# Performance work log

Measured on AMD Instinct MI355X. Metric: run time of the kernel, lower is better.

## Reference

```python
import jax, jax.numpy as jnp
import numpy as np

N_NODES = 100000
N_EDGES = 1250000
NUM_RELS = 8
D_IN, D_HID, D_OUT = 64, 64, 32


def setup_inputs() -> dict:
    key = jax.random.key(0)
    ks = jax.random.split(key, 10)
    x = jax.random.normal(ks[0], (N_NODES, D_IN), dtype=jnp.float32)
    src = jax.random.randint(ks[1], (N_EDGES,), 0, N_NODES, dtype=jnp.int32)
    dst = jax.random.randint(ks[2], (N_EDGES,), 0, N_NODES, dtype=jnp.int32)
    edge_type = jax.random.randint(ks[3], (N_EDGES,), 0, NUM_RELS, dtype=jnp.int32)
    s1 = 1.0 / np.sqrt(D_IN)
    s2 = 1.0 / np.sqrt(D_HID)
    W1 = jax.random.uniform(ks[4], (NUM_RELS, D_IN, D_HID), jnp.float32, -s1, s1)
    root1 = jax.random.uniform(ks[5], (D_IN, D_HID), jnp.float32, -s1, s1)
    b1 = jnp.zeros((D_HID,), jnp.float32)
    W2 = jax.random.uniform(ks[6], (NUM_RELS, D_HID, D_OUT), jnp.float32, -s2, s2)
    root2 = jax.random.uniform(ks[7], (D_HID, D_OUT), jnp.float32, -s2, s2)
    b2 = jnp.zeros((D_OUT,), jnp.float32)
    return {"x": x, "W1": W1, "root1": root1, "b1": b1,
            "W2": W2, "root2": root2, "b2": b2,
            "src": src, "dst": dst, "edge_type": edge_type}


def rgcn_conv(x, W, root, b, src, dst, edge_type, num_rels, num_nodes):
    # self-loop (root) transform + bias
    out = x @ root + b
    for r in range(num_rels):  # loop over small fixed relation set
        mask = (edge_type == r).astype(x.dtype)          # (E,)
        h = x @ W[r]                                      # (N, dout): transform once per relation
        msg = h[src] * mask[:, None]                      # (E, dout) gather + mask
        agg = jax.ops.segment_sum(msg, dst, num_segments=num_nodes)
        cnt = jax.ops.segment_sum(mask, dst, num_segments=num_nodes)
        out = out + agg / jnp.maximum(cnt, 1.0)[:, None]  # per-relation mean (PyG default aggr)
    return out


def reference(x, W1, root1, b1, W2, root2, b2, src, dst, edge_type):
    h = jax.nn.relu(rgcn_conv(x, W1, root1, b1, src, dst, edge_type, NUM_RELS, N_NODES))
    return rgcn_conv(h, W2, root2, b2, src, dst, edge_type, NUM_RELS, N_NODES)
```

## Files before the change

### kernel.cpp

```cpp
#include <hip/hip_runtime.h>

typedef _Float16 half8 __attribute__((ext_vector_type(8)));
typedef __attribute__((ext_vector_type(4))) float f32x4;

__device__ __forceinline__ unsigned short f2h(float f) {
    _Float16 h = (_Float16)f;
    return *(unsigned short*)&h;
}
__device__ __forceinline__ float h2f(unsigned short u) {
    _Float16 h = *(_Float16*)&u;
    return (float)h;
}


__device__ __forceinline__ void wprep_body(
    const float* __restrict__ W, const float* __restrict__ root,
    unsigned short* __restrict__ wb, int dout, int idx)
{
    int c = idx / (64 * dout);
    int rme = idx % (64 * dout);
    int kk = rme / dout;
    int j = rme % dout;
    float f = (c == 0) ? root[kk * dout + j]
                       : W[(size_t)(c - 1) * 64 * dout + kk * dout + j];
    wb[(size_t)c * dout * 72 + (size_t)j * 72 + kk] = f2h(f);
}

__global__ __launch_bounds__(256) void prep_kernel(
    const float* __restrict__ x, unsigned short* __restrict__ xh, int n8,
    const float* __restrict__ W1, const float* __restrict__ root1,
    unsigned short* __restrict__ wb1,
    const float* __restrict__ W2, const float* __restrict__ root2,
    unsigned short* __restrict__ wb2,
    int* __restrict__ hist, int nhist4)
{
    int id = blockIdx.x * 256 + threadIdx.x;
    if (id < n8) {
        const f32x4* p = (const f32x4*)(x + (size_t)id * 8);
        f32x4 u = p[0], v = p[1];
        half8 o;
#pragma unroll
        for (int j = 0; j < 4; ++j) {
            o[j] = (_Float16)u[j];
            o[j + 4] = (_Float16)v[j];
        }
        *(half8*)(xh + (size_t)id * 8) = o;
        return;
    }
    id -= n8;
    if (id < 9 * 64 * 64) { wprep_body(W1, root1, wb1, 64, id); return; }
    id -= 9 * 64 * 64;
    if (id < 9 * 64 * 32) { wprep_body(W2, root2, wb2, 32, id); return; }
    id -= 9 * 64 * 32;
    if (id < nhist4) ((int4*)hist)[id] = make_int4(0, 0, 0, 0);
}


__global__ __launch_bounds__(256) void hist8_kernel(
    const int* __restrict__ dst, const int* __restrict__ et,
    int* __restrict__ hist, int E)
{
    int e = blockIdx.x * 256 + threadIdx.x;
    if (e < E) atomicAdd(&hist[dst[e] * 8 + et[e]], 1);
}

#define SCAN_TILE 4096
__global__ __launch_bounds__(1024) void scanA_kernel(
    const int* __restrict__ hist, int* __restrict__ bstart,
    int* __restrict__ partial, int nkeys)
{
    __shared__ int wsum[16];
    const int t = threadIdx.x;
    const int lane = t & 63, w = t >> 6;
    const int base = blockIdx.x * SCAN_TILE + t * 4;
    int v[4];
    int s = 0;
#pragma unroll
    for (int i = 0; i < 4; ++i) {
        v[i] = (base + i < nkeys) ? hist[base + i] : 0;
        s += v[i];
    }
    int inc = s;
#pragma unroll
    for (int off = 1; off < 64; off <<= 1) {
        int u = __shfl_up(inc, off);
        if (lane >= off) inc += u;
    }
    if (lane == 63) wsum[w] = inc;
    __syncthreads();
    if (w == 0 && lane < 16) {
        int ws = wsum[lane];
        int winc = ws;
#pragma unroll
        for (int off = 1; off < 16; off <<= 1) {
            int u = __shfl_up(winc, off);
            if (lane >= off) winc += u;
        }
        wsum[lane] = winc - ws;
    }
    __syncthreads();
    int run = wsum[w] + (inc - s);
#pragma unroll
    for (int i = 0; i < 4; ++i) {
        if (base + i < nkeys) bstart[base + i] = run;
        run += v[i];
    }
    if (t == 1023) partial[blockIdx.x] = run;
}

__global__ __launch_bounds__(64) void scanB_kernel(
    const int* __restrict__ partial, int* __restrict__ pscan,
    int* __restrict__ bstart_end, int nblk)
{
    const int lane = threadIdx.x;
    int running = 0;
    for (int b = 0; b < nblk; b += 64) {
        int i = b + lane;
        int o = (i < nblk) ? partial[i] : 0;
        int v = o;
#pragma unroll
        for (int off = 1; off < 64; off <<= 1) {
            int u = __shfl_up(v, off);
            if (lane >= off) v += u;
        }
        if (i < nblk) pscan[i] = running + v - o;
        running += __shfl(v, 63);
    }
    if (lane == 0) *bstart_end = running;
}

__global__ __launch_bounds__(256) void scatter_kernel(
    const int* __restrict__ src, const int* __restrict__ dst,
    const int* __restrict__ et, int* __restrict__ hist,
    const int* __restrict__ bstart, const int* __restrict__ pscan,
    unsigned* __restrict__ srt, int E)
{
    int e = blockIdx.x * 256 + threadIdx.x;
    if (e < E) {
        int key = dst[e] * 8 + et[e];
        int r = atomicSub(&hist[key], 1) - 1;
        srt[bstart[key] + pscan[key >> 12] + r] = (unsigned)src[e];
    }
}


template <int DOUT, int RELU, int OUTH>
__global__ __launch_bounds__(256, 6) void fused_kernel(
    const unsigned short* __restrict__ tab,
    const unsigned* __restrict__ srt,
    const int* __restrict__ bstart,
    const int* __restrict__ pscan,
    const unsigned short* __restrict__ wb,
    const float* __restrict__ bias,
    float* __restrict__ outf,
    unsigned short* __restrict__ outh,
    int n_nodes, int Etot)
{
    __shared__ __align__(16) unsigned short Atile[16 * 600];

    const int t = threadIdx.x;
    const int w = t >> 6, lane = t & 63;
    const int quad = lane >> 4, l16 = lane & 15;
    const int nbt = blockIdx.x * 16;
    const int nb4 = nbt + w * 4;
    const int KEYS = n_nodes * 8;

    {
        const int nb0 = nb4 * 8;
        int idx = nb0 + lane; if (idx > KEYS) idx = KEYS;
        int lv;
        if (idx < KEYS) lv = bstart[idx] + pscan[idx >> 12];
        else            lv = Etot;
        const int E0 = __builtin_amdgcn_readlane(lv, 0);
        const int E1 = __builtin_amdgcn_readlane(lv, 32);

        int cntv = __shfl_down(lv, 1) - lv;
        float rsc = 1.0f / fmaxf((float)cntv, 1.0f);

#pragma unroll
        for (int i = 0; i < 4; ++i) {
            int node = nb4 + i;
            unsigned short v = 0;
            if (node < n_nodes) v = tab[(size_t)node * 64 + lane];
            Atile[(w * 4 + i) * 600 + lane] = v;
        }

        float acc0 = 0.f, acc1 = 0.f;
        int R = 0;
        int bnext = __builtin_amdgcn_readlane(lv, 1);

        auto flushes = [&](int eabs) {
            while (R < 32 && eabs == bnext) {
                float sc = __uint_as_float(
                    __builtin_amdgcn_readlane(__float_as_uint(rsc), R));
                Atile[(w * 4 + (R >> 3)) * 600 + 64 + (R & 7) * 64 + lane] =
                    f2h((acc0 + acc1) * sc);
                acc0 = 0.f; acc1 = 0.f;
                ++R;
                bnext = (R < 31) ? __builtin_amdgcn_readlane(lv, R + 1) : E1;
            }
        };

        const char* tabc = (const char*)tab;
        const unsigned voff = (unsigned)(lane << 1);
        unsigned GA[16], GB[16];

#define ISSUE16(BUF, RECV, KB)                                              \
        _Pragma("unroll")                                                   \
        for (int i_ = 0; i_ < 16; ++i_) {                                   \
            int q_ = __builtin_amdgcn_readlane((int)(RECV), (KB) + i_);     \
            const char* ap_ = tabc + ((size_t)(unsigned)q_ << 7);           \
            asm volatile("global_load_ushort %0, %1, %2"                    \
                         : "=v"(BUF[i_]) : "v"(voff), "s"(ap_));            \
        }
#define WAIT16  asm volatile("s_waitcnt vmcnt(16)" ::: "memory")
#define WAIT0   asm volatile("s_waitcnt vmcnt(0)" ::: "memory")
#define SB      __builtin_amdgcn_sched_barrier(0)
#define CONSUME_FULL(BUF, B)                                                \
        _Pragma("unroll")                                                   \
        for (int i_ = 0; i_ < 16; ++i_) {                                   \
            flushes(base + (B) + i_);                                       \
            if (i_ & 1) acc1 += h2f((unsigned short)BUF[i_]);               \
            else        acc0 += h2f((unsigned short)BUF[i_]);               \
        }
#define CONSUME_TAIL(BUF, B)                                                \
        _Pragma("unroll")                                                   \
        for (int i_ = 0; i_ < 16; ++i_) {                                   \
            if ((B) + i_ < blen) {                                          \
                flushes(base + (B) + i_);                                   \
                if (i_ & 1) acc1 += h2f((unsigned short)BUF[i_]);           \
                else        acc0 += h2f((unsigned short)BUF[i_]);           \
            }                                                               \
        }

        int base = E0;
        unsigned rec = 0;
        if (base < E1 && lane < E1 - base) rec = srt[base + lane];
        while (base < E1) {
            const int blen = min(64, E1 - base);
            const int nbase = base + 64;
            unsigned recn = 0;
            if (nbase < E1) {
                int ei = nbase + lane;
                if (ei > E1 - 1) ei = E1 - 1;
                unsigned eoff = (unsigned)ei << 2;
                asm volatile("global_load_dword %0, %1, %2"
                             : "=v"(recn) : "v"(eoff), "s"(srt));
            }

            const bool m1 = blen > 16, m2 = blen > 32, m3 = blen > 48;
            ISSUE16(GA, rec, 0);
            if (m1) { ISSUE16(GB, rec, 16); WAIT16; } else WAIT0;
            SB;
            if (blen >= 16) { CONSUME_FULL(GA, 0); } else { CONSUME_TAIL(GA, 0); }
            if (m1) {
                if (m2) { ISSUE16(GA, rec, 32); WAIT16; } else WAIT0;
                SB;
                if (blen >= 32) { CONSUME_FULL(GB, 16); } else { CONSUME_TAIL(GB, 16); }
            }
            if (m2) {
                if (m3) { ISSUE16(GB, rec, 48); WAIT16; } else WAIT0;
                SB;
                if (blen >= 48) { CONSUME_FULL(GA, 32); } else { CONSUME_TAIL(GA, 32); }
            }
            if (m3) {
                WAIT0;
                SB;
                if (blen >= 64) { CONSUME_FULL(GB, 48); } else { CONSUME_TAIL(GB, 48); }
            }
            base = nbase;
            rec = recn;
        }
#undef ISSUE16
#undef WAIT16
#undef WAIT0
#undef SB
#undef CONSUME_FULL
#undef CONSUME_TAIL
        flushes(E1);
        while (R < 32) {
            float sc = __uint_as_float(
                __builtin_amdgcn_readlane(__float_as_uint(rsc), R));
            Atile[(w * 4 + (R >> 3)) * 600 + 64 + (R & 7) * 64 + lane] =
                f2h((acc0 + acc1) * sc);
            acc0 = 0.f; acc1 = 0.f;
            ++R;
        }
    }

    __syncthreads();

    constexpr int JPW = DOUT / 16;
    if (JPW == 2 && w >= 2) return;

    const int j = w * 16 + l16;
    f32x4 d = {0.f, 0.f, 0.f, 0.f};
    const unsigned short* arow = &Atile[l16 * 600];
#pragma unroll
    for (int c = 0; c < 9; ++c) {
        half8 a0 = *(const half8*)(arow + c * 64 + quad * 8);
        half8 a1 = *(const half8*)(arow + c * 64 + 32 + quad * 8);
        half8 b0 = *(const half8*)&wb[c * DOUT * 72 + j * 72 + quad * 8];
        half8 b1 = *(const half8*)&wb[c * DOUT * 72 + j * 72 + 32 + quad * 8];
        d = __builtin_amdgcn_mfma_f32_16x16x32_f16(a0, b0, d, 0, 0, 0);
        d = __builtin_amdgcn_mfma_f32_16x16x32_f16(a1, b1, d, 0, 0, 0);
    }

    const float bj = bias[j];
#pragma unroll
    for (int r = 0; r < 4; ++r) {
        const int node = nbt + quad * 4 + r;
        if (node < n_nodes) {
            float v = d[r] + bj;
            if (RELU) v = fmaxf(v, 0.0f);
            if (OUTH) outh[(size_t)node * 64 + j] = f2h(v);
            else      outf[(size_t)node * DOUT + j] = v;
        }
    }
}

extern "C" void kernel_launch(void* const* d_in, const int* in_sizes, int n_in,
                              void* d_out, int out_size, void* d_ws, size_t ws_size,
                              hipStream_t stream) {
    const float* x     = (const float*)d_in[0];
    const float* W1    = (const float*)d_in[1];
    const float* root1 = (const float*)d_in[2];
    const float* b1    = (const float*)d_in[3];
    const float* W2    = (const float*)d_in[4];
    const float* root2 = (const float*)d_in[5];
    const float* b2    = (const float*)d_in[6];
    const int*   src   = (const int*)d_in[7];
    const int*   dst   = (const int*)d_in[8];
    const int*   et    = (const int*)d_in[9];

    const int N = in_sizes[0] / 64;
    const int E = in_sizes[7];
    const int KEYS = N * 8;

    char* p = (char*)d_ws;
    auto alloc = [&](size_t bytes) {
        char* r = p;
        p += (bytes + 15) & ~(size_t)15;
        return r;
    };
    unsigned* srt       = (unsigned*)alloc((size_t)E * 4);
    int* hist           = (int*)alloc((size_t)KEYS * 4);
    int* bstart         = (int*)alloc((size_t)(KEYS + 1) * 4);
    int* partial        = (int*)alloc(256 * 4);
    int* pscan          = (int*)alloc(256 * 4);
    unsigned short* wb1 = (unsigned short*)alloc((size_t)9 * 64 * 72 * 2);
    unsigned short* wb2 = (unsigned short*)alloc((size_t)9 * 32 * 72 * 2);
    unsigned short* xh  = (unsigned short*)alloc((size_t)N * 64 * 2);
    unsigned short* h   = (unsigned short*)alloc((size_t)N * 64 * 2);

    const int n8 = N * 8;
    const int nhist4 = KEYS / 4;
    const int prep_items = n8 + 9 * 64 * 64 + 9 * 64 * 32 + nhist4;
    prep_kernel<<<(prep_items + 255) / 256, 256, 0, stream>>>(
        x, xh, n8, W1, root1, wb1, W2, root2, wb2, hist, nhist4);

    hist8_kernel<<<(E + 255) / 256, 256, 0, stream>>>(dst, et, hist, E);
    const int nscan = (KEYS + SCAN_TILE - 1) / SCAN_TILE;
    scanA_kernel<<<nscan, 1024, 0, stream>>>(hist, bstart, partial, KEYS);
    scanB_kernel<<<1, 64, 0, stream>>>(partial, pscan, bstart + KEYS, nscan);
    scatter_kernel<<<(E + 255) / 256, 256, 0, stream>>>(
        src, dst, et, hist, bstart, pscan, srt, E);

    fused_kernel<64, 1, 1><<<(N + 15) / 16, 256, 0, stream>>>(
        xh, srt, bstart, pscan, wb1, b1, nullptr, h, N, E);
    fused_kernel<32, 0, 0><<<(N + 15) / 16, 256, 0, stream>>>(
        h, srt, bstart, pscan, wb2, b2, (float*)d_out, nullptr, N, E);
}
```

Before: 354.7 us.

## Gather neighbor rows via global_load_lds into double-buffered LDS staging

Replaces the per-edge 2-byte global_load_ushort gathers into registers with 4-byte global_load_lds direct-to-LDS loads, where each instruction fetches two neighbor rows (one per half-wave). Rows land in a per-wave double-buffered shared staging area and are read back from LDS for accumulation. The aim is to halve the number of gather instructions and free VGPRs. In exchange it adds LDS traffic and 16 KB of shared memory per block, and lowers the occupancy hint from 6 to 4 blocks.

```diff
diff --git a/kernel.cpp b/kernel.cpp
--- a/kernel.cpp
+++ b/kernel.cpp
@@ -145,7 +145,7 @@
 
 
 template <int DOUT, int RELU, int OUTH>
-__global__ __launch_bounds__(256, 6) void fused_kernel(
+__global__ __launch_bounds__(256, 4) void fused_kernel(
     const unsigned short* __restrict__ tab,
     const unsigned* __restrict__ srt,
     const int* __restrict__ bstart,
@@ -157,6 +157,7 @@
     int n_nodes, int Etot)
 {
     __shared__ __align__(16) unsigned short Atile[16 * 600];
+    __shared__ __align__(16) unsigned char SBUF[4][2][2048];
 
     const int t = threadIdx.x;
     const int w = t >> 6, lane = t & 63;
@@ -202,39 +203,26 @@
         };
 
         const char* tabc = (const char*)tab;
-        const unsigned voff = (unsigned)(lane << 1);
-        unsigned GA[16], GB[16];
-
-#define ISSUE16(BUF, RECV, KB)                                              \
-        _Pragma("unroll")                                                   \
-        for (int i_ = 0; i_ < 16; ++i_) {                                   \
-            int q_ = __builtin_amdgcn_readlane((int)(RECV), (KB) + i_);     \
-            const char* ap_ = tabc + ((size_t)(unsigned)q_ << 7);           \
-            asm volatile("global_load_ushort %0, %1, %2"                    \
-                         : "=v"(BUF[i_]) : "v"(voff), "s"(ap_));            \
-        }
-#define WAIT16  asm volatile("s_waitcnt vmcnt(16)" ::: "memory")
-#define WAIT0   asm volatile("s_waitcnt vmcnt(0)" ::: "memory")
-#define SB      __builtin_amdgcn_sched_barrier(0)
-#define CONSUME_FULL(BUF, B)                                                \
-        _Pragma("unroll")                                                   \
-        for (int i_ = 0; i_ < 16; ++i_) {                                   \
-            flushes(base + (B) + i_);                                       \
-            if (i_ & 1) acc1 += h2f((unsigned short)BUF[i_]);               \
-            else        acc0 += h2f((unsigned short)BUF[i_]);               \
-        }
-#define CONSUME_TAIL(BUF, B)                                                \
-        _Pragma("unroll")                                                   \
-        for (int i_ = 0; i_ < 16; ++i_) {                                   \
-            if ((B) + i_ < blen) {                                          \
-                flushes(base + (B) + i_);                                   \
-                if (i_ & 1) acc1 += h2f((unsigned short)BUF[i_]);           \
-                else        acc0 += h2f((unsigned short)BUF[i_]);           \
-            }                                                               \
-        }
+        const unsigned loff = (unsigned)(lane & 31) << 2;
+        unsigned rec = 0;
+
+        auto issue8 = [&](int buf, int kb) {
+#pragma unroll
+            for (int s = 0; s < 8; ++s) {
+                int qlo = __builtin_amdgcn_readlane((int)rec, kb + 2 * s);
+                int qhi = __builtin_amdgcn_readlane((int)rec, kb + 2 * s + 1);
+                const char* rl = tabc + ((size_t)(unsigned)qlo << 7);
+                const char* rh = tabc + ((size_t)(unsigned)qhi << 7);
+                const char* gp = ((lane < 32) ? rl : rh) + loff;
+                __builtin_amdgcn_global_load_lds(
+                    (const __attribute__((address_space(1))) unsigned*)gp,
+                    (__attribute__((address_space(3))) unsigned*)
+                        &SBUF[w][buf][s * 256],
+                    4, 0, 0);
+            }
+        };
 
         int base = E0;
-        unsigned rec = 0;
         if (base < E1 && lane < E1 - base) rec = srt[base + lane];
         while (base < E1) {
             const int blen = min(64, E1 - base);
@@ -248,35 +236,31 @@
                              : "=v"(recn) : "v"(eoff), "s"(srt));
             }
 
-            const bool m1 = blen > 16, m2 = blen > 32, m3 = blen > 48;
-            ISSUE16(GA, rec, 0);
-            if (m1) { ISSUE16(GB, rec, 16); WAIT16; } else WAIT0;
-            SB;
-            if (blen >= 16) { CONSUME_FULL(GA, 0); } else { CONSUME_TAIL(GA, 0); }
-            if (m1) {
-                if (m2) { ISSUE16(GA, rec, 32); WAIT16; } else WAIT0;
-                SB;
-                if (blen >= 32) { CONSUME_FULL(GB, 16); } else { CONSUME_TAIL(GB, 16); }
-            }
-            if (m2) {
-                if (m3) { ISSUE16(GB, rec, 48); WAIT16; } else WAIT0;
-                SB;
-                if (blen >= 48) { CONSUME_FULL(GA, 32); } else { CONSUME_TAIL(GA, 32); }
-            }
-            if (m3) {
-                WAIT0;
-                SB;
-                if (blen >= 64) { CONSUME_FULL(GB, 48); } else { CONSUME_TAIL(GB, 48); }
+            int buf = 0;
+            issue8(0, 0);
+            for (int B = 0; B < blen; B += 16) {
+                if (B + 16 < blen) {
+                    issue8(buf ^ 1, B + 16);
+                    asm volatile("s_waitcnt vmcnt(8)" ::: "memory");
+                } else {
+                    asm volatile("s_waitcnt vmcnt(0)" ::: "memory");
+                }
+                __builtin_amdgcn_sched_barrier(0);
+                const unsigned short* sb =
+                    (const unsigned short*)&SBUF[w][buf][0];
+#pragma unroll
+                for (int s = 0; s < 8; ++s) {
+                    const int e = B + 2 * s;
+                    float vlo = h2f(sb[s * 128 + lane]);
+                    float vhi = h2f(sb[s * 128 + 64 + lane]);
+                    if (e < blen)     { flushes(base + e);     acc0 += vlo; }
+                    if (e + 1 < blen) { flushes(base + e + 1); acc1 += vhi; }
+                }
+                buf ^= 1;
             }
             base = nbase;
             rec = recn;
         }
-#undef ISSUE16
-#undef WAIT16
-#undef WAIT0
-#undef SB
-#undef CONSUME_FULL
-#undef CONSUME_TAIL
         flushes(E1);
         while (R < 32) {
             float sc = __uint_as_float(
```

Result: slower. 396.4 us (+11.8%).
